# Kernel tuning notes

Hardware: AMD Instinct MI355X
Metric: run time of the kernel (lower is better)

The kernel has to match this reference:

```python
import jax, jax.numpy as jnp
import numpy as np

DEG = np.pi / 180.0
H_FOV = (-180.0 * DEG, 180.0 * DEG)   # azimuth fov (rad)
V_FOV = (-3.0 * DEG, 25.0 * DEG)      # elevation fov (rad), phi = -asin(z/r)
W = 2048  # int((h_fov[1]-h_fov[0]) / h_res), h_res = 360/2048 deg
H = 64    # int((v_fov[1]-v_fov[0]) / v_res), v_res = 28/64 deg
B = 8
N = 2_000_000


def setup_inputs() -> dict:
    key = jax.random.key(0)
    k1, k2, k3 = jax.random.split(key, 3)
    # realistic lidar-scale coordinates: wide xy spread, shallow z
    xyz = jax.random.normal(k1, (N, 3), jnp.float32) * jnp.array([30.0, 30.0, 3.0], jnp.float32)
    inten = jax.random.uniform(k2, (N, 1), dtype=jnp.float32)
    bs = jax.random.randint(k3, (N, 1), 0, B).astype(jnp.float32)  # batch idx stored as float col 0
    points = jnp.concatenate([bs, xyz, inten], axis=1)  # [N, 5]
    return {"points": points, "batch_size": B}


def reference(points, batch_size):
    # points: [N, 1+4] = (batch_idx, x, y, z, intensity)
    bs_idx = points[:, 0].astype(jnp.int32)
    xyz = points[:, 1:4]
    extra = points[:, 4:]

    # spherical projection: r, theta (azimuth, cw from +x), phi (elevation, cw from xy-plane)
    r = jnp.linalg.norm(xyz, axis=1, keepdims=True)                      # [N,1]
    theta = -jnp.arctan2(xyz[:, 1], xyz[:, 0])[:, None]                  # [N,1]
    phi = -jnp.arcsin(xyz[:, 2:3] / jnp.maximum(r, 1e-5))                # [N,1]

    u_n = (theta - H_FOV[0]) / (H_FOV[1] - H_FOV[0])                     # [N,1] normed col
    v_n = (phi - V_FOV[0]) / (V_FOV[1] - V_FOV[0])                       # [N,1] normed row

    mask = (u_n[:, 0] >= 0) & (u_n[:, 0] < 1) & (v_n[:, 0] >= 0) & (v_n[:, 0] < 1)

    u = (u_n[:, 0] * W).astype(jnp.int32)
    v = (v_n[:, 0] * H).astype(jnp.int32)
    # route masked-out points to an out-of-bounds index; scatter mode='drop' discards them
    u = jnp.where(mask, u, W)
    v = jnp.where(mask, v, H)

    # use_xyz=True: features = [xyz, rThetaPhi, raw_features] -> channels = 7
    features = jnp.concatenate([xyz, r, theta, phi, extra], axis=1)      # [N,7]

    rv = jnp.zeros((batch_size, H, W, features.shape[1]), points.dtype)
    rv = rv.at[bs_idx, v, u].set(features, mode='drop')
    return jnp.transpose(rv, (0, 3, 1, 2))  # [B, 7, H, W]
```

## Files before the change

kernel.cpp:

```cpp
#include <hip/hip_runtime.h>
#include <math.h>

#define W_IMG 2048
#define H_IMG 64
#define B_IMG 8
#define C_IMG 7
#define HW_IMG (H_IMG * W_IMG)
#define NPIX (B_IMG * HW_IMG)

__device__ __forceinline__ float F(unsigned u) { return __uint_as_float(u); }
#define FMAF(a,b,c) __builtin_fmaf((a),(b),(c))

__device__ __forceinline__ float glibc_atanf(float x) {
    const float atanhi[4] = {F(0x3eed6338u), F(0x3f490fdau), F(0x3f7b985eu), F(0x3fc90fdau)};
    const float atanlo[4] = {F(0x31ac3769u), F(0x33222168u), F(0x33140fb4u), F(0x33a22168u)};
    const float aT0 = F(0x3eaaaaabu), aT1 = F(0xbe4ccccdu), aT2 = F(0x3e124925u),
                aT3 = F(0xbde38e38u), aT4 = F(0x3dba2e6eu), aT5 = F(0xbd9d8795u),
                aT6 = F(0x3d886b35u), aT7 = F(0xbd6ef16bu), aT8 = F(0x3d4bda59u),
                aT9 = F(0xbd15a221u), aT10 = F(0x3c8569d7u);

    unsigned hx = __float_as_uint(x);
    unsigned ix = hx & 0x7fffffffu;
    if (ix >= 0x4c800000u) {
        if (ix > 0x7f800000u) return x + x;
        float v = __fadd_rn(atanhi[3], atanlo[3]);
        return (hx >> 31) ? -v : v;
    }
    int id;
    float xr = x;
    if (ix < 0x3ee00000u) {
        if (ix < 0x31000000u) return x;
        id = -1;
    } else {
        xr = fabsf(x);
        if (ix < 0x3f980000u) {
            if (ix < 0x3f300000u) {
                id = 0;
                xr = __fdiv_rn(__fsub_rn(__fmul_rn(2.0f, xr), 1.0f),
                               __fadd_rn(2.0f, xr));
            } else {
                id = 1;
                xr = __fdiv_rn(__fsub_rn(xr, 1.0f), __fadd_rn(xr, 1.0f));
            }
        } else {
            if (ix < 0x401c0000u) {
                id = 2;
                xr = __fdiv_rn(__fsub_rn(xr, 1.5f),
                               __fadd_rn(1.0f, __fmul_rn(1.5f, xr)));
            } else {
                id = 3;
                xr = __fdiv_rn(-1.0f, xr);
            }
        }
    }
    float z = __fmul_rn(xr, xr);
    float w = __fmul_rn(z, z);
    float s1 = __fmul_rn(z, __fadd_rn(aT0, __fmul_rn(w, __fadd_rn(aT2,
               __fmul_rn(w, __fadd_rn(aT4, __fmul_rn(w, __fadd_rn(aT6,
               __fmul_rn(w, __fadd_rn(aT8, __fmul_rn(w, aT10)))))))))));
    float s2 = __fmul_rn(w, __fadd_rn(aT1, __fmul_rn(w, __fadd_rn(aT3,
               __fmul_rn(w, __fadd_rn(aT5, __fmul_rn(w, __fadd_rn(aT7,
               __fmul_rn(w, aT9)))))))));
    if (id < 0) return __fsub_rn(x, __fmul_rn(x, __fadd_rn(s1, s2)));
    float zz = __fsub_rn(atanhi[id],
               __fsub_rn(__fsub_rn(__fmul_rn(xr, __fadd_rn(s1, s2)), atanlo[id]), xr));
    return (hx >> 31) ? -zz : zz;
}

__device__ __forceinline__ float glibc_atan2f(float y, float x) {
    const float pi_o_2 = F(0x3fc90fdbu);
    const float pi     = F(0x40490fdbu);
    const float pi_lo  = F(0xb3bbbd2eu);
    unsigned hx = __float_as_uint(x), hy = __float_as_uint(y);
    unsigned ix = hx & 0x7fffffffu, iy = hy & 0x7fffffffu;
    if (ix > 0x7f800000u || iy > 0x7f800000u) return x + y;
    if (hx == 0x3f800000u) return glibc_atanf(y);
    unsigned m = ((hy >> 31) & 1u) | ((hx >> 30) & 2u);
    if (iy == 0) {
        switch (m) {
            case 0: case 1: return y;
            case 2: return pi;
            default: return -pi;
        }
    }
    if (ix == 0) return (m & 1u) ? -pi_o_2 : pi_o_2;
    if (ix == 0x7f800000u) {
        if (iy == 0x7f800000u) {
            switch (m) {
                case 0: return F(0x3f490fdbu);
                case 1: return -F(0x3f490fdbu);
                case 2: return __fmul_rn(3.0f, F(0x3f490fdbu));
                default: return -__fmul_rn(3.0f, F(0x3f490fdbu));
            }
        } else {
            switch (m) {
                case 0: return 0.0f;
                case 1: return -0.0f;
                case 2: return pi;
                default: return -pi;
            }
        }
    }
    if (iy == 0x7f800000u) return (m & 1u) ? -pi_o_2 : pi_o_2;

    int k = ((int)iy - (int)ix) >> 23;
    float z;
    if (k > 26) {
        z = __fadd_rn(pi_o_2, __fmul_rn(0.5f, pi_lo));
        m &= 1u;
    } else if (k < -26 && (hx >> 31)) {
        z = 0.0f;
    } else {
        z = glibc_atanf(fabsf(__fdiv_rn(y, x)));
    }
    switch (m) {
        case 0: return z;
        case 1: return __uint_as_float(__float_as_uint(z) ^ 0x80000000u);
        case 2: return __fsub_rn(pi, __fsub_rn(z, pi_lo));
        default: return __fsub_rn(__fsub_rn(z, pi_lo), pi);
    }
}

struct Proj {
    float theta, phi;
    int   pix;
    bool  in_image;
};

__device__ __forceinline__ Proj project_from(float x, float y, float zr, float bsf) {
    const float H0F   = (float)(-3.14159265358979323846);
    const float SPANH = (float)( 6.28318530717958647692);
    const float V0F   = (float)(-3.0 * 3.14159265358979323846 / 180.0);
    const float SPANV = (float)((25.0 * 3.14159265358979323846 / 180.0) -
                                (-3.0 * 3.14159265358979323846 / 180.0));
    const float RH = 1.0f / SPANH;
    const float RV = 1.0f / SPANV;

    Proj p;
    p.theta = -glibc_atan2f(y, x);
    float s  = __fsqrt_rn(FMAF(-zr, zr, 1.0f));
    float d  = __fadd_rn(1.0f, s);
    p.phi = -__fmul_rn(2.0f, glibc_atan2f(zr, d));

    float u_n = __fmul_rn(__fsub_rn(p.theta, H0F), RH);
    float v_n = __fmul_rn(__fsub_rn(p.phi,   V0F), RV);
    p.in_image = (u_n >= 0.0f) && (u_n < 1.0f) && (v_n >= 0.0f) && (v_n < 1.0f);
    p.pix = -1;
    if (p.in_image) {
        int u = (int)__fmul_rn(u_n, (float)W_IMG);
        int v = (int)__fmul_rn(v_n, (float)H_IMG);
        int b = (int)bsf;
        if (u < W_IMG && v < H_IMG) {
            p.pix = (b * H_IMG + v) * W_IMG + u;
        } else {
            p.in_image = false;
        }
    }
    return p;
}

__device__ __forceinline__ float norm_r(float x, float y, float z) {
    return __fsqrt_rn(FMAF(z, z, FMAF(y, y, __fmul_rn(x, x))));
}

__global__ void init_winner(int4* winner4, int n4) {
    int i = blockIdx.x * blockDim.x + threadIdx.x;
    if (i < n4) winner4[i] = make_int4(-1, -1, -1, -1);
}

__global__ void scatter_winner(const float* __restrict__ pts, int* __restrict__ winner, int n) {
    int t  = blockIdx.x * blockDim.x + threadIdx.x;
    int i0 = t * 4;
    if (i0 >= n) return;

    float bx[4], px[4], py[4], pz[4];
    if (i0 + 4 <= n) {
        const float4* p4 = (const float4*)(pts + (size_t)i0 * 5);
        float4 c0 = p4[0], c1 = p4[1], c2 = p4[2], c3 = p4[3], c4 = p4[4];
        bx[0] = c0.x; px[0] = c0.y; py[0] = c0.z; pz[0] = c0.w;
        bx[1] = c1.y; px[1] = c1.z; py[1] = c1.w; pz[1] = c2.x;
        bx[2] = c2.z; px[2] = c2.w; py[2] = c3.x; pz[2] = c3.y;
        bx[3] = c3.w; px[3] = c4.x; py[3] = c4.y; pz[3] = c4.z;
    } else {
        for (int k = 0; k < 4; ++k) {
            int i = i0 + k;
            if (i < n) {
                const float* q = pts + (size_t)i * 5;
                bx[k] = q[0]; px[k] = q[1]; py[k] = q[2]; pz[k] = q[3];
            } else {
                bx[k] = 0.f; px[k] = 0.f; py[k] = 0.f; pz[k] = 1e9f;
            }
        }
    }
#pragma unroll
    for (int k = 0; k < 4; ++k) {
        float x = px[k], y = py[k], z = pz[k];
        float r  = norm_r(x, y, z);
        float zr = __fdiv_rn(z, fmaxf(r, 1e-5f));
        if (zr > 0.05240f || zr < -0.42270f) continue;
        Proj p = project_from(x, y, zr, bx[k]);
        if (p.in_image) {
            atomicMax(&winner[p.pix], i0 + k);
        }
    }
}

__global__ void write_output(const float* __restrict__ pts, const int* __restrict__ winner,
                             float* __restrict__ out) {
    int t  = blockIdx.x * blockDim.x + threadIdx.x;
    int p0 = t * 4;
    if (p0 >= NPIX) return;

    int4 w4 = *(const int4*)(winner + p0);
    int wis[4] = {w4.x, w4.y, w4.z, w4.w};

    float qb[4], qx[4], qy[4], qz[4], qi[4];
#pragma unroll
    for (int k = 0; k < 4; ++k) {
        if (wis[k] >= 0) {
            const float* q = pts + (size_t)wis[k] * 5;
            qb[k] = q[0]; qx[k] = q[1]; qy[k] = q[2]; qz[k] = q[3]; qi[k] = q[4];
        }
    }

    float fc[C_IMG][4];
#pragma unroll
    for (int c = 0; c < C_IMG; ++c)
#pragma unroll
        for (int k = 0; k < 4; ++k) fc[c][k] = 0.f;

#pragma unroll
    for (int k = 0; k < 4; ++k) {
        if (wis[k] >= 0) {
            float x = qx[k], y = qy[k], z = qz[k];
            float r  = norm_r(x, y, z);
            float zr = __fdiv_rn(z, fmaxf(r, 1e-5f));
            Proj pr = project_from(x, y, zr, qb[k]);
            fc[0][k] = x; fc[1][k] = y; fc[2][k] = z;
            fc[3][k] = r; fc[4][k] = pr.theta; fc[5][k] = pr.phi;
            fc[6][k] = qi[k];
        }
    }

    int b  = p0 >> 17;
    int hw = p0 & (HW_IMG - 1);
    size_t base = (size_t)b * C_IMG * HW_IMG + hw;
#pragma unroll
    for (int c = 0; c < C_IMG; ++c) {
        float4 v = make_float4(fc[c][0], fc[c][1], fc[c][2], fc[c][3]);
        *(float4*)(out + base + (size_t)c * HW_IMG) = v;
    }
}

extern "C" void kernel_launch(void* const* d_in, const int* in_sizes, int n_in,
                              void* d_out, int out_size, void* d_ws, size_t ws_size,
                              hipStream_t stream) {
    const float* pts = (const float*)d_in[0];
    int n = in_sizes[0] / 5;
    int* winner = (int*)d_ws;
    float* out = (float*)d_out;

    int n4 = NPIX / 4;
    init_winner<<<(n4 + 255) / 256, 256, 0, stream>>>((int4*)winner, n4);

    int nthreads = (n + 3) / 4;
    scatter_winner<<<(nthreads + 255) / 256, 256, 0, stream>>>(pts, winner, n);

    int pthreads = NPIX / 4;
    write_output<<<(pthreads + 255) / 256, 256, 0, stream>>>(pts, winner, out);
}
```

Measured before the change: 157.8 us.

## Scatter points in reverse order with pre-check to skip losing atomics

```diff
diff --git a/kernel.cpp b/kernel.cpp
--- a/kernel.cpp
+++ b/kernel.cpp
@@ -7,6 +7,8 @@
 #define C_IMG 7
 #define HW_IMG (H_IMG * W_IMG)
 #define NPIX (B_IMG * HW_IMG)
+
+typedef float v4f __attribute__((ext_vector_type(4)));
 
 __device__ __forceinline__ float F(unsigned u) { return __uint_as_float(u); }
 #define FMAF(a,b,c) __builtin_fmaf((a),(b),(c))
@@ -168,45 +170,28 @@
     if (i < n4) winner4[i] = make_int4(-1, -1, -1, -1);
 }
 
-__global__ void scatter_winner(const float* __restrict__ pts, int* __restrict__ winner, int n) {
-    int t  = blockIdx.x * blockDim.x + threadIdx.x;
-    int i0 = t * 4;
-    if (i0 >= n) return;
-
-    float bx[4], px[4], py[4], pz[4];
-    if (i0 + 4 <= n) {
-        const float4* p4 = (const float4*)(pts + (size_t)i0 * 5);
-        float4 c0 = p4[0], c1 = p4[1], c2 = p4[2], c3 = p4[3], c4 = p4[4];
-        bx[0] = c0.x; px[0] = c0.y; py[0] = c0.z; pz[0] = c0.w;
-        bx[1] = c1.y; px[1] = c1.z; py[1] = c1.w; pz[1] = c2.x;
-        bx[2] = c2.z; px[2] = c2.w; py[2] = c3.x; pz[2] = c3.y;
-        bx[3] = c3.w; px[3] = c4.x; py[3] = c4.y; pz[3] = c4.z;
-    } else {
-        for (int k = 0; k < 4; ++k) {
-            int i = i0 + k;
-            if (i < n) {
-                const float* q = pts + (size_t)i * 5;
-                bx[k] = q[0]; px[k] = q[1]; py[k] = q[2]; pz[k] = q[3];
-            } else {
-                bx[k] = 0.f; px[k] = 0.f; py[k] = 0.f; pz[k] = 1e9f;
-            }
-        }
-    }
-#pragma unroll
-    for (int k = 0; k < 4; ++k) {
-        float x = px[k], y = py[k], z = pz[k];
-        float r  = norm_r(x, y, z);
-        float zr = __fdiv_rn(z, fmaxf(r, 1e-5f));
-        if (zr > 0.05240f || zr < -0.42270f) continue;
-        Proj p = project_from(x, y, zr, bx[k]);
-        if (p.in_image) {
-            atomicMax(&winner[p.pix], i0 + k);
-        }
-    }
-}
-
-__global__ void write_output(const float* __restrict__ pts, const int* __restrict__ winner,
-                             float* __restrict__ out) {
+__global__ void __launch_bounds__(256, 8)
+scatter_winner(const float* __restrict__ pts, int* __restrict__ winner, int n) {
+    int t = blockIdx.x * blockDim.x + threadIdx.x;
+    if (t >= n) return;
+    int i = n - 1 - t;
+    const float* q = pts + (size_t)i * 5;
+    float bsf = q[0], x = q[1], y = q[2], z = q[3];
+
+    float r  = norm_r(x, y, z);
+    float zr = __fdiv_rn(z, fmaxf(r, 1e-5f));
+    if (zr > 0.05240f || zr < -0.42270f) return;
+
+    Proj p = project_from(x, y, zr, bsf);
+    if (!p.in_image) return;
+
+    if (winner[p.pix] >= i) return;
+    atomicMax(&winner[p.pix], i);
+}
+
+__global__ void __launch_bounds__(256, 4)
+write_output(const float* __restrict__ pts, const int* __restrict__ winner,
+             float* __restrict__ out) {
     int t  = blockIdx.x * blockDim.x + threadIdx.x;
     int p0 = t * 4;
     if (p0 >= NPIX) return;
@@ -247,8 +232,8 @@
     size_t base = (size_t)b * C_IMG * HW_IMG + hw;
 #pragma unroll
     for (int c = 0; c < C_IMG; ++c) {
-        float4 v = make_float4(fc[c][0], fc[c][1], fc[c][2], fc[c][3]);
-        *(float4*)(out + base + (size_t)c * HW_IMG) = v;
+        v4f v = {fc[c][0], fc[c][1], fc[c][2], fc[c][3]};
+        __builtin_nontemporal_store(v, (v4f*)(out + base + (size_t)c * HW_IMG));
     }
 }
 
@@ -263,8 +248,7 @@
     int n4 = NPIX / 4;
     init_winner<<<(n4 + 255) / 256, 256, 0, stream>>>((int4*)winner, n4);
 
-    int nthreads = (n + 3) / 4;
-    scatter_winner<<<(nthreads + 255) / 256, 256, 0, stream>>>(pts, winner, n);
+    scatter_winner<<<(n + 255) / 256, 256, 0, stream>>>(pts, winner, n);
 
     int pthreads = NPIX / 4;
     write_output<<<(pthreads + 255) / 256, 256, 0, stream>>>(pts, winner, out);
```

Measured after the change: 149.6 us. 5.2% less time.
